# Kernel tuning notes

Measured on AMD Instinct MI355X. Metric: run time of the kernel, lower is better.

Reference implementation:

```python
import jax, jax.numpy as jnp
import numpy as np

CLIP_LIMIT = 10.0
NTILES = 8        # OpenCV createCLAHE default tileGridSize=(8,8)
NBINS = 256

_M_RGB2XYZ = jnp.array([[0.412453, 0.357580, 0.180423],
                        [0.212671, 0.715160, 0.072169],
                        [0.019334, 0.119193, 0.950227]], dtype=jnp.float32)
_M_XYZ2RGB = jnp.array([[ 3.240479, -1.537150, -0.498535],
                        [-0.969256,  1.875992,  0.041556],
                        [ 0.055648, -0.204043,  1.057311]], dtype=jnp.float32)
_WP = jnp.array([0.950456, 1.0, 1.088754], dtype=jnp.float32)  # D65 white point (OpenCV)
_EPS = 0.008856


def rgb2lab(rgb):  # rgb: [H,W,3] in [0,1]
    xyz = jnp.einsum('hwc,dc->hwd', rgb, _M_RGB2XYZ) / _WP
    f = jnp.where(xyz > _EPS, jnp.cbrt(xyz), 7.787 * xyz + 16.0 / 116.0)
    fx, fy, fz = f[..., 0], f[..., 1], f[..., 2]
    L = 116.0 * fy - 16.0
    a = 500.0 * (fx - fy)
    b = 200.0 * (fy - fz)
    return L, a, b


def lab2rgb(L, a, b):
    fy = (L + 16.0) / 116.0
    fx = fy + a / 500.0
    fz = fy - b / 200.0
    f = jnp.stack([fx, fy, fz], axis=-1)
    xyz = jnp.where(f ** 3 > _EPS, f ** 3, (f - 16.0 / 116.0) / 7.787) * _WP
    rgb = jnp.einsum('hwd,cd->hwc', xyz, _M_XYZ2RGB)
    return jnp.clip(rgb, 0.0, 1.0)


def clahe_channel(L8, clip_limit):
    # L8: [H,W] int32 in [0,255]
    H, W = L8.shape
    th, tw = H // NTILES, W // NTILES
    area = float(th * tw)
    # per-tile histograms via one scatter-add
    rows = jnp.arange(H) // th            # [H] tile row id
    cols = jnp.arange(W) // tw            # [W] tile col id
    tid = rows[:, None] * NTILES + cols[None, :]          # [H,W]
    flat = (tid * NBINS + L8).ravel()
    hist = jnp.zeros(NTILES * NTILES * NBINS, jnp.float32).at[flat].add(1.0)
    hist = hist.reshape(NTILES * NTILES, NBINS)
    # clip + uniform redistribution of excess
    clip = max(clip_limit * area / NBINS, 1.0)
    excess = jnp.sum(jnp.maximum(hist - clip, 0.0), axis=1, keepdims=True)
    hist = jnp.minimum(hist, clip) + excess / NBINS
    # CDF -> LUT (OpenCV: lutScale = 255/tileArea, rounded)
    cdf = jnp.cumsum(hist, axis=1)
    lut = jnp.clip(jnp.round(cdf * (255.0 / area)), 0.0, 255.0)  # [T, 256]
    # bilinear interpolation between tile LUTs
    fy = jnp.clip((jnp.arange(H, dtype=jnp.float32) + 0.5) / th - 0.5, 0.0, NTILES - 1.0)
    fx = jnp.clip((jnp.arange(W, dtype=jnp.float32) + 0.5) / tw - 0.5, 0.0, NTILES - 1.0)
    y0 = jnp.floor(fy).astype(jnp.int32); y1 = jnp.minimum(y0 + 1, NTILES - 1)
    x0 = jnp.floor(fx).astype(jnp.int32); x1 = jnp.minimum(x0 + 1, NTILES - 1)
    wy = (fy - y0)[:, None]; wx = (fx - x0)[None, :]
    def g(yi, xi):  # gather LUT value for each pixel from tile (yi, xi)
        return lut[yi[:, None] * NTILES + xi[None, :], L8]
    top = (1.0 - wx) * g(y0, x0) + wx * g(y0, x1)
    bot = (1.0 - wx) * g(y1, x0) + wx * g(y1, x1)
    return (1.0 - wy) * top + wy * bot   # [H,W] float in [0,255]


def setup_inputs() -> dict:
    key = jax.random.key(0)
    x = jax.random.uniform(key, (3, 2048, 2048), dtype=jnp.float32)
    return {"x": x}


def reference(x) -> jnp.ndarray:
    hwc = jnp.transpose(x, (1, 2, 0))          # CHW -> HWC
    L, a, b = rgb2lab(hwc)                      # L in [0,100]
    L8 = jnp.clip(jnp.round(L * (255.0 / 100.0)), 0, 255).astype(jnp.int32)
    L_eq = clahe_channel(L8, CLIP_LIMIT) * (100.0 / 255.0)
    rgb = lab2rgb(L_eq, a, b)
    return jnp.transpose(rgb, (2, 0, 1))        # HWC -> CHW
```

## Files before the change

### kernel.cpp

```cpp
#include <hip/hip_runtime.h>
#include <stdint.h>

#define HW 4194304
#define WIDTH 2048
#define F(x) ((float)(x))

__device__ __forceinline__ float cbrtf_glibc(float x) {
    unsigned int bits = __float_as_uint(x);
    int xe = (int)((bits >> 23) & 0xFF) - 126;
    float xm = __uint_as_float((bits & 0x007FFFFFu) | 0x3F000000u);

    static const double factor[5] = {
        1.0 / 1.5874010519681994748,
        1.0 / 1.2599210498948731648,
        1.0,
        1.2599210498948731648,
        1.5874010519681994748
    };

    double xmd = (double)xm;
    double p = __dsub_rn(0.697570460207922770, __dmul_rn(0.191502161678719066, xmd));
    p = __dadd_rn(0.492659620528969547, __dmul_rn(p, xmd));
    float u = (float)p;

    float t2 = __fmul_rn(__fmul_rn(u, u), u);

    double ud  = (double)u;
    double t2d = (double)t2;
    double num = __dmul_rn(ud, __dadd_rn(t2d, __dmul_rn(2.0, xmd)));
    double den = __dadd_rn(__dmul_rn(2.0, t2d), xmd);
    double ym  = __dmul_rn(__ddiv_rn(num, den), factor[2 + (xe % 3)]);
    float ymf = (float)ym;

    return ldexpf(ymf, xe / 3);
}

__device__ __forceinline__ void rgb2lab_px(float r, float g, float b,
                                           int& l8, float& A_, float& B_) {
    float X = __fadd_rn(__fadd_rn(__fmul_rn(r, F(0.412453)), __fmul_rn(g, F(0.357580))), __fmul_rn(b, F(0.180423)));
    float Y = __fadd_rn(__fadd_rn(__fmul_rn(r, F(0.212671)), __fmul_rn(g, F(0.715160))), __fmul_rn(b, F(0.072169)));
    float Z = __fadd_rn(__fadd_rn(__fmul_rn(r, F(0.019334)), __fmul_rn(g, F(0.119193))), __fmul_rn(b, F(0.950227)));
    X = __fdiv_rn(X, F(0.950456));
    Z = __fdiv_rn(Z, F(1.088754));
    const float EPS = F(0.008856);
    const float C0  = F(16.0 / 116.0);
    float fx = (X > EPS) ? cbrtf_glibc(X) : __fadd_rn(__fmul_rn(F(7.787), X), C0);
    float fy = (Y > EPS) ? cbrtf_glibc(Y) : __fadd_rn(__fmul_rn(F(7.787), Y), C0);
    float fz = (Z > EPS) ? cbrtf_glibc(Z) : __fadd_rn(__fmul_rn(F(7.787), Z), C0);
    float L  = __fsub_rn(__fmul_rn(F(116.0), fy), F(16.0));
    A_ = __fmul_rn(F(500.0), __fsub_rn(fx, fy));
    B_ = __fmul_rn(F(200.0), __fsub_rn(fy, fz));
    float Lr = rintf(__fmul_rn(L, F(255.0 / 100.0)));
    Lr = fminf(fmaxf(Lr, 0.0f), 255.0f);
    l8 = (int)Lr;
}

__device__ __forceinline__ int l8_of_rgb(float r, float g, float b) {
    float Y = __fadd_rn(__fadd_rn(__fmul_rn(r, F(0.212671)), __fmul_rn(g, F(0.715160))), __fmul_rn(b, F(0.072169)));
    const float EPS = F(0.008856);
    const float C0  = F(16.0 / 116.0);
    float fy = (Y > EPS) ? cbrtf_glibc(Y) : __fadd_rn(__fmul_rn(F(7.787), Y), C0);
    float L  = __fsub_rn(__fmul_rn(F(116.0), fy), F(16.0));
    float Lr = rintf(__fmul_rn(L, F(255.0 / 100.0)));
    Lr = fminf(fmaxf(Lr, 0.0f), 255.0f);
    return (int)Lr;
}

__device__ __forceinline__ void lab2rgb_px(float Leq, float A_, float B_,
                                           float& rr, float& gg, float& bb) {
    const float EPS = F(0.008856);
    const float C0  = F(16.0 / 116.0);
    float fy2 = __fdiv_rn(__fadd_rn(Leq, 16.0f), 116.0f);
    float fx2 = __fadd_rn(fy2, __fdiv_rn(A_, 500.0f));
    float fz2 = __fsub_rn(fy2, __fdiv_rn(B_, 200.0f));
    float t3;
    t3 = fx2 * fx2 * fx2;
    float X = ((t3 > EPS) ? t3 : __fdiv_rn(__fsub_rn(fx2, C0), F(7.787))) * F(0.950456);
    t3 = fy2 * fy2 * fy2;
    float Y = ((t3 > EPS) ? t3 : __fdiv_rn(__fsub_rn(fy2, C0), F(7.787))) * F(1.0);
    t3 = fz2 * fz2 * fz2;
    float Z = ((t3 > EPS) ? t3 : __fdiv_rn(__fsub_rn(fz2, C0), F(7.787))) * F(1.088754);
    rr = __fadd_rn(__fadd_rn(__fmul_rn(X, F(3.240479)),  __fmul_rn(Y, F(-1.537150))), __fmul_rn(Z, F(-0.498535)));
    gg = __fadd_rn(__fadd_rn(__fmul_rn(X, F(-0.969256)), __fmul_rn(Y, F(1.875992))),  __fmul_rn(Z, F(0.041556)));
    bb = __fadd_rn(__fadd_rn(__fmul_rn(X, F(0.055648)),  __fmul_rn(Y, F(-0.204043))), __fmul_rn(Z, F(1.057311)));
    rr = fminf(fmaxf(rr, 0.0f), 1.0f);
    gg = fminf(fmaxf(gg, 0.0f), 1.0f);
    bb = fminf(fmaxf(bb, 0.0f), 1.0f);
}

__global__ __launch_bounds__(256, 4) void k_histY(const float* __restrict__ x,
                                                  unsigned int* __restrict__ hist) {
    __shared__ unsigned int h[2048];
    const int t = threadIdx.x;
    const int y = blockIdx.x;
    #pragma unroll
    for (int i = 0; i < 8; ++i) h[i * 256 + t] = 0;
    __syncthreads();

    const int base = y * WIDTH + t * 8;
    float4 ra = *(const float4*)(x + base);
    float4 rb = *(const float4*)(x + base + 4);
    float4 ga = *(const float4*)(x + base + HW);
    float4 gb = *(const float4*)(x + base + HW + 4);
    float4 ba = *(const float4*)(x + base + 2 * HW);
    float4 bb = *(const float4*)(x + base + 2 * HW + 4);

    const int hb = ((t >> 5) << 8);
    atomicAdd(&h[hb + l8_of_rgb(ra.x, ga.x, ba.x)], 1u);
    atomicAdd(&h[hb + l8_of_rgb(ra.y, ga.y, ba.y)], 1u);
    atomicAdd(&h[hb + l8_of_rgb(ra.z, ga.z, ba.z)], 1u);
    atomicAdd(&h[hb + l8_of_rgb(ra.w, ga.w, ba.w)], 1u);
    atomicAdd(&h[hb + l8_of_rgb(rb.x, gb.x, bb.x)], 1u);
    atomicAdd(&h[hb + l8_of_rgb(rb.y, gb.y, bb.y)], 1u);
    atomicAdd(&h[hb + l8_of_rgb(rb.z, gb.z, bb.z)], 1u);
    atomicAdd(&h[hb + l8_of_rgb(rb.w, gb.w, bb.w)], 1u);

    __syncthreads();
    unsigned int* gh = hist + (y >> 8) * 2048;
    #pragma unroll
    for (int i = 0; i < 8; ++i) {
        unsigned int v = h[i * 256 + t];
        if (v) atomicAdd(&gh[i * 256 + t], v);
    }
}

__global__ __launch_bounds__(256, 4) void k_lut_apply(const float* __restrict__ x,
        const unsigned int* __restrict__ hist,
        float* __restrict__ out) {
    __shared__ float lutS[4096];
    const int t = threadIdx.x;
    const int y = blockIdx.x;

    float fyc = fminf(fmaxf(((float)y + 0.5f) * (1.0f / 256.0f) - 0.5f, 0.0f), 7.0f);
    int y0 = (int)floorf(fyc);
    int y1 = min(y0 + 1, 7);
    float wy = __fsub_rn(fyc, (float)y0);
    float omwy = __fsub_rn(1.0f, wy);

    {
        const int lane = t & 63;
        const int w = t >> 6;
        #pragma unroll
        for (int i = 0; i < 4; ++i) {
            int gidx = w * 4 + i;
            int trow = gidx >> 3;
            int tcol = gidx & 7;
            int tile = (trow ? y1 : y0) * 8 + tcol;
            uint4 hv = *(const uint4*)(hist + tile * 256 + lane * 4);
            float h0 = (float)hv.x, h1 = (float)hv.y, h2 = (float)hv.z, h3 = (float)hv.w;
            float e = __fadd_rn(__fadd_rn(fmaxf(h0 - 2560.0f, 0.0f),
                                          fmaxf(h1 - 2560.0f, 0.0f)),
                                __fadd_rn(fmaxf(h2 - 2560.0f, 0.0f),
                                          fmaxf(h3 - 2560.0f, 0.0f)));
            #pragma unroll
            for (int d = 1; d < 64; d <<= 1) e = __fadd_rn(e, __shfl_xor(e, d));
            float ex = __fmul_rn(e, F(1.0 / 256.0));
            float v0 = __fadd_rn(fminf(h0, 2560.0f), ex);
            float v1 = __fadd_rn(fminf(h1, 2560.0f), ex);
            float v2 = __fadd_rn(fminf(h2, 2560.0f), ex);
            float v3 = __fadd_rn(fminf(h3, 2560.0f), ex);
            float s0 = v0;
            float s1 = __fadd_rn(s0, v1);
            float s2 = __fadd_rn(s1, v2);
            float s3 = __fadd_rn(s2, v3);
            float sc = s3;
            #pragma unroll
            for (int d = 1; d < 64; d <<= 1) {
                float u2 = __shfl_up(sc, d);
                if (lane >= d) sc = __fadd_rn(sc, u2);
            }
            float excl = __fsub_rn(sc, s3);
            int lb = trow * 2048 + tcol * 256 + lane * 4;
            float c0 = rintf(__fmul_rn(__fadd_rn(excl, s0), F(255.0 / 65536.0)));
            float c1 = rintf(__fmul_rn(__fadd_rn(excl, s1), F(255.0 / 65536.0)));
            float c2 = rintf(__fmul_rn(__fadd_rn(excl, s2), F(255.0 / 65536.0)));
            float c3 = rintf(__fmul_rn(__fadd_rn(excl, s3), F(255.0 / 65536.0)));
            lutS[lb + 0] = fminf(fmaxf(c0, 0.0f), 255.0f);
            lutS[lb + 1] = fminf(fmaxf(c1, 0.0f), 255.0f);
            lutS[lb + 2] = fminf(fmaxf(c2, 0.0f), 255.0f);
            lutS[lb + 3] = fminf(fmaxf(c3, 0.0f), 255.0f);
        }
    }
    __syncthreads();

    const int colbase = t * 8;
    const int base = y * WIDTH + colbase;
    float4 ra = *(const float4*)(x + base);
    float4 rb = *(const float4*)(x + base + 4);
    float4 ga = *(const float4*)(x + base + HW);
    float4 gb = *(const float4*)(x + base + HW + 4);
    float4 ba = *(const float4*)(x + base + 2 * HW);
    float4 bb = *(const float4*)(x + base + 2 * HW + 4);

    float4 o_r0, o_r1, o_g0, o_g1, o_b0, o_b1;

#define PIX(RV, GV, BV, J, OR_, OG_, OB_) {                                       \
    int col = colbase + (J);                                                      \
    int l8; float A_, B_;                                                         \
    rgb2lab_px((RV), (GV), (BV), l8, A_, B_);                                     \
    float fxc = fminf(fmaxf(((float)col + 0.5f) * (1.0f / 256.0f) - 0.5f, 0.0f), 7.0f); \
    int x0 = (int)floorf(fxc);                                                    \
    int x1 = min(x0 + 1, 7);                                                      \
    float wx = __fsub_rn(fxc, (float)x0);                                         \
    float omwx = __fsub_rn(1.0f, wx);                                             \
    float g00 = lutS[x0 * 256 + l8];                                              \
    float g01 = lutS[x1 * 256 + l8];                                              \
    float g10 = lutS[2048 + x0 * 256 + l8];                                       \
    float g11 = lutS[2048 + x1 * 256 + l8];                                       \
    float top_ = __fadd_rn(__fmul_rn(omwx, g00), __fmul_rn(wx, g01));             \
    float bot_ = __fadd_rn(__fmul_rn(omwx, g10), __fmul_rn(wx, g11));             \
    float Leq = __fmul_rn(__fadd_rn(__fmul_rn(omwy, top_), __fmul_rn(wy, bot_)),  \
                          F(100.0 / 255.0));                                      \
    lab2rgb_px(Leq, A_, B_, (OR_), (OG_), (OB_));                                 \
}

    PIX(ra.x, ga.x, ba.x, 0, o_r0.x, o_g0.x, o_b0.x);
    PIX(ra.y, ga.y, ba.y, 1, o_r0.y, o_g0.y, o_b0.y);
    PIX(ra.z, ga.z, ba.z, 2, o_r0.z, o_g0.z, o_b0.z);
    PIX(ra.w, ga.w, ba.w, 3, o_r0.w, o_g0.w, o_b0.w);
    PIX(rb.x, gb.x, bb.x, 4, o_r1.x, o_g1.x, o_b1.x);
    PIX(rb.y, gb.y, bb.y, 5, o_r1.y, o_g1.y, o_b1.y);
    PIX(rb.z, gb.z, bb.z, 6, o_r1.z, o_g1.z, o_b1.z);
    PIX(rb.w, gb.w, bb.w, 7, o_r1.w, o_g1.w, o_b1.w);
#undef PIX

    *(float4*)(out + base)              = o_r0;
    *(float4*)(out + base + 4)          = o_r1;
    *(float4*)(out + base + HW)         = o_g0;
    *(float4*)(out + base + HW + 4)     = o_g1;
    *(float4*)(out + base + 2 * HW)     = o_b0;
    *(float4*)(out + base + 2 * HW + 4) = o_b1;
}

extern "C" void kernel_launch(void* const* d_in, const int* in_sizes, int n_in,
                              void* d_out, int out_size, void* d_ws, size_t ws_size,
                              hipStream_t stream) {
    const float* x = (const float*)d_in[0];
    float* out = (float*)d_out;
    unsigned int* hist = (unsigned int*)d_ws;

    (void)hipMemsetAsync(hist, 0, 65536, stream);
    k_histY<<<2048, 256, 0, stream>>>(x, hist);
    k_lut_apply<<<2048, 256, 0, stream>>>(x, hist, out);
}
```

Baseline: 141.8 us.

## Cache Lab a/b and L8 from histogram pass for reuse in apply pass

```diff
diff --git a/kernel.cpp b/kernel.cpp
--- a/kernel.cpp
+++ b/kernel.cpp
@@ -53,17 +53,6 @@
     float Lr = rintf(__fmul_rn(L, F(255.0 / 100.0)));
     Lr = fminf(fmaxf(Lr, 0.0f), 255.0f);
     l8 = (int)Lr;
-}
-
-__device__ __forceinline__ int l8_of_rgb(float r, float g, float b) {
-    float Y = __fadd_rn(__fadd_rn(__fmul_rn(r, F(0.212671)), __fmul_rn(g, F(0.715160))), __fmul_rn(b, F(0.072169)));
-    const float EPS = F(0.008856);
-    const float C0  = F(16.0 / 116.0);
-    float fy = (Y > EPS) ? cbrtf_glibc(Y) : __fadd_rn(__fmul_rn(F(7.787), Y), C0);
-    float L  = __fsub_rn(__fmul_rn(F(116.0), fy), F(16.0));
-    float Lr = rintf(__fmul_rn(L, F(255.0 / 100.0)));
-    Lr = fminf(fmaxf(Lr, 0.0f), 255.0f);
-    return (int)Lr;
 }
 
 __device__ __forceinline__ void lab2rgb_px(float Leq, float A_, float B_,
@@ -88,8 +77,10 @@
     bb = fminf(fmaxf(bb, 0.0f), 1.0f);
 }
 
-__global__ __launch_bounds__(256, 4) void k_histY(const float* __restrict__ x,
-                                                  unsigned int* __restrict__ hist) {
+__global__ __launch_bounds__(256, 8) void k_hist_ab(const float* __restrict__ x,
+        unsigned int* __restrict__ hist,
+        float* __restrict__ Abuf, float* __restrict__ Bbuf,
+        unsigned int* __restrict__ l8buf, int store) {
     __shared__ unsigned int h[2048];
     const int t = threadIdx.x;
     const int y = blockIdx.x;
@@ -97,24 +88,32 @@
     for (int i = 0; i < 8; ++i) h[i * 256 + t] = 0;
     __syncthreads();
 
-    const int base = y * WIDTH + t * 8;
-    float4 ra = *(const float4*)(x + base);
-    float4 rb = *(const float4*)(x + base + 4);
-    float4 ga = *(const float4*)(x + base + HW);
-    float4 gb = *(const float4*)(x + base + HW + 4);
-    float4 ba = *(const float4*)(x + base + 2 * HW);
-    float4 bb = *(const float4*)(x + base + 2 * HW + 4);
-
-    const int hb = ((t >> 5) << 8);
-    atomicAdd(&h[hb + l8_of_rgb(ra.x, ga.x, ba.x)], 1u);
-    atomicAdd(&h[hb + l8_of_rgb(ra.y, ga.y, ba.y)], 1u);
-    atomicAdd(&h[hb + l8_of_rgb(ra.z, ga.z, ba.z)], 1u);
-    atomicAdd(&h[hb + l8_of_rgb(ra.w, ga.w, ba.w)], 1u);
-    atomicAdd(&h[hb + l8_of_rgb(rb.x, gb.x, bb.x)], 1u);
-    atomicAdd(&h[hb + l8_of_rgb(rb.y, gb.y, bb.y)], 1u);
-    atomicAdd(&h[hb + l8_of_rgb(rb.z, gb.z, bb.z)], 1u);
-    atomicAdd(&h[hb + l8_of_rgb(rb.w, gb.w, bb.w)], 1u);
-
+    const int rowbase = y * WIDTH;
+    #pragma unroll
+    for (int ch = 0; ch < 2; ++ch) {
+        const int col0 = ch * 1024 + 4 * t;
+        const int idx  = rowbase + col0;
+        float4 r4 = *(const float4*)(x + idx);
+        float4 g4 = *(const float4*)(x + idx + HW);
+        float4 b4 = *(const float4*)(x + idx + 2 * HW);
+        int l80, l81, l82, l83;
+        float A0, A1, A2, A3, B0, B1, B2, B3;
+        rgb2lab_px(r4.x, g4.x, b4.x, l80, A0, B0);
+        rgb2lab_px(r4.y, g4.y, b4.y, l81, A1, B1);
+        rgb2lab_px(r4.z, g4.z, b4.z, l82, A2, B2);
+        rgb2lab_px(r4.w, g4.w, b4.w, l83, A3, B3);
+        const int hb = (col0 >> 8) << 8;
+        atomicAdd(&h[hb + l80], 1u);
+        atomicAdd(&h[hb + l81], 1u);
+        atomicAdd(&h[hb + l82], 1u);
+        atomicAdd(&h[hb + l83], 1u);
+        if (store) {
+            *(float4*)(Abuf + idx) = make_float4(A0, A1, A2, A3);
+            *(float4*)(Bbuf + idx) = make_float4(B0, B1, B2, B3);
+            l8buf[idx >> 2] = (unsigned)l80 | ((unsigned)l81 << 8)
+                            | ((unsigned)l82 << 16) | ((unsigned)l83 << 24);
+        }
+    }
     __syncthreads();
     unsigned int* gh = hist + (y >> 8) * 2048;
     #pragma unroll
@@ -124,9 +123,11 @@
     }
 }
 
-__global__ __launch_bounds__(256, 4) void k_lut_apply(const float* __restrict__ x,
+__global__ __launch_bounds__(256, 8) void k_lut_apply(const float* __restrict__ x,
         const unsigned int* __restrict__ hist,
-        float* __restrict__ out) {
+        const float* __restrict__ Abuf, const float* __restrict__ Bbuf,
+        const unsigned int* __restrict__ l8buf,
+        float* __restrict__ out, int stored) {
     __shared__ float lutS[4096];
     const int t = threadIdx.x;
     const int y = blockIdx.x;
@@ -183,53 +184,60 @@
     }
     __syncthreads();
 
-    const int colbase = t * 8;
-    const int base = y * WIDTH + colbase;
-    float4 ra = *(const float4*)(x + base);
-    float4 rb = *(const float4*)(x + base + 4);
-    float4 ga = *(const float4*)(x + base + HW);
-    float4 gb = *(const float4*)(x + base + HW + 4);
-    float4 ba = *(const float4*)(x + base + 2 * HW);
-    float4 bb = *(const float4*)(x + base + 2 * HW + 4);
-
-    float4 o_r0, o_r1, o_g0, o_g1, o_b0, o_b1;
-
-#define PIX(RV, GV, BV, J, OR_, OG_, OB_) {                                       \
-    int col = colbase + (J);                                                      \
-    int l8; float A_, B_;                                                         \
-    rgb2lab_px((RV), (GV), (BV), l8, A_, B_);                                     \
+    const int rowbase = y * WIDTH;
+    #pragma unroll
+    for (int ch = 0; ch < 2; ++ch) {
+        const int col0 = ch * 1024 + 4 * t;
+        const int idx  = rowbase + col0;
+        float A0, A1, A2, A3, B0, B1, B2, B3;
+        int l80, l81, l82, l83;
+        if (stored) {
+            float4 a4 = *(const float4*)(Abuf + idx);
+            float4 b4 = *(const float4*)(Bbuf + idx);
+            unsigned p = l8buf[idx >> 2];
+            A0 = a4.x; A1 = a4.y; A2 = a4.z; A3 = a4.w;
+            B0 = b4.x; B1 = b4.y; B2 = b4.z; B3 = b4.w;
+            l80 = (int)(p & 0xFFu); l81 = (int)((p >> 8) & 0xFFu);
+            l82 = (int)((p >> 16) & 0xFFu); l83 = (int)((p >> 24) & 0xFFu);
+        } else {
+            float4 r4 = *(const float4*)(x + idx);
+            float4 g4 = *(const float4*)(x + idx + HW);
+            float4 b4 = *(const float4*)(x + idx + 2 * HW);
+            rgb2lab_px(r4.x, g4.x, b4.x, l80, A0, B0);
+            rgb2lab_px(r4.y, g4.y, b4.y, l81, A1, B1);
+            rgb2lab_px(r4.z, g4.z, b4.z, l82, A2, B2);
+            rgb2lab_px(r4.w, g4.w, b4.w, l83, A3, B3);
+        }
+
+        float4 o_r, o_g, o_b;
+
+#define PIX(J, L8V, AV, BV, OR_, OG_, OB_) {                                      \
+    int col = col0 + (J);                                                         \
     float fxc = fminf(fmaxf(((float)col + 0.5f) * (1.0f / 256.0f) - 0.5f, 0.0f), 7.0f); \
-    int x0 = (int)floorf(fxc);                                                    \
-    int x1 = min(x0 + 1, 7);                                                      \
-    float wx = __fsub_rn(fxc, (float)x0);                                         \
+    int xi0 = (int)floorf(fxc);                                                   \
+    int xi1 = min(xi0 + 1, 7);                                                    \
+    float wx = __fsub_rn(fxc, (float)xi0);                                        \
     float omwx = __fsub_rn(1.0f, wx);                                             \
-    float g00 = lutS[x0 * 256 + l8];                                              \
-    float g01 = lutS[x1 * 256 + l8];                                              \
-    float g10 = lutS[2048 + x0 * 256 + l8];                                       \
-    float g11 = lutS[2048 + x1 * 256 + l8];                                       \
+    float g00 = lutS[xi0 * 256 + (L8V)];                                          \
+    float g01 = lutS[xi1 * 256 + (L8V)];                                          \
+    float g10 = lutS[2048 + xi0 * 256 + (L8V)];                                   \
+    float g11 = lutS[2048 + xi1 * 256 + (L8V)];                                   \
     float top_ = __fadd_rn(__fmul_rn(omwx, g00), __fmul_rn(wx, g01));             \
     float bot_ = __fadd_rn(__fmul_rn(omwx, g10), __fmul_rn(wx, g11));             \
     float Leq = __fmul_rn(__fadd_rn(__fmul_rn(omwy, top_), __fmul_rn(wy, bot_)),  \
                           F(100.0 / 255.0));                                      \
-    lab2rgb_px(Leq, A_, B_, (OR_), (OG_), (OB_));                                 \
-}
-
-    PIX(ra.x, ga.x, ba.x, 0, o_r0.x, o_g0.x, o_b0.x);
-    PIX(ra.y, ga.y, ba.y, 1, o_r0.y, o_g0.y, o_b0.y);
-    PIX(ra.z, ga.z, ba.z, 2, o_r0.z, o_g0.z, o_b0.z);
-    PIX(ra.w, ga.w, ba.w, 3, o_r0.w, o_g0.w, o_b0.w);
-    PIX(rb.x, gb.x, bb.x, 4, o_r1.x, o_g1.x, o_b1.x);
-    PIX(rb.y, gb.y, bb.y, 5, o_r1.y, o_g1.y, o_b1.y);
-    PIX(rb.z, gb.z, bb.z, 6, o_r1.z, o_g1.z, o_b1.z);
-    PIX(rb.w, gb.w, bb.w, 7, o_r1.w, o_g1.w, o_b1.w);
+    lab2rgb_px(Leq, (AV), (BV), (OR_), (OG_), (OB_));                             \
+}
+        PIX(0, l80, A0, B0, o_r.x, o_g.x, o_b.x);
+        PIX(1, l81, A1, B1, o_r.y, o_g.y, o_b.y);
+        PIX(2, l82, A2, B2, o_r.z, o_g.z, o_b.z);
+        PIX(3, l83, A3, B3, o_r.w, o_g.w, o_b.w);
 #undef PIX
 
-    *(float4*)(out + base)              = o_r0;
-    *(float4*)(out + base + 4)          = o_r1;
-    *(float4*)(out + base + HW)         = o_g0;
-    *(float4*)(out + base + HW + 4)     = o_g1;
-    *(float4*)(out + base + 2 * HW)     = o_b0;
-    *(float4*)(out + base + 2 * HW + 4) = o_b1;
+        *(float4*)(out + idx)          = o_r;
+        *(float4*)(out + idx + HW)     = o_g;
+        *(float4*)(out + idx + 2 * HW) = o_b;
+    }
 }
 
 extern "C" void kernel_launch(void* const* d_in, const int* in_sizes, int n_in,
@@ -237,9 +245,16 @@
                               hipStream_t stream) {
     const float* x = (const float*)d_in[0];
     float* out = (float*)d_out;
-    unsigned int* hist = (unsigned int*)d_ws;
+    char* ws = (char*)d_ws;
+    unsigned int* hist = (unsigned int*)ws;
+    const size_t off = 131072;
+    float* Abuf = (float*)(ws + off);
+    float* Bbuf = (float*)(ws + off + (size_t)HW * 4);
+    unsigned int* l8buf = (unsigned int*)(ws + off + (size_t)HW * 8);
+    const size_t need = off + (size_t)HW * 9;
+    const int store = (ws_size >= need) ? 1 : 0;
 
     (void)hipMemsetAsync(hist, 0, 65536, stream);
-    k_histY<<<2048, 256, 0, stream>>>(x, hist);
-    k_lut_apply<<<2048, 256, 0, stream>>>(x, hist, out);
-}
+    k_hist_ab<<<2048, 256, 0, stream>>>(x, hist, Abuf, Bbuf, l8buf, store);
+    k_lut_apply<<<2048, 256, 0, stream>>>(x, hist, Abuf, Bbuf, l8buf, out, store);
+}
```

Measured after the change: 132.8 us. 6.4% less time.
